# Optimization experiments

Hardware: AMD Instinct MI355X
Metric: run time of the kernel (lower is better)

The kernel has to match this reference:

```python
import math
import jax
import jax.numpy as jnp
import numpy as np

B, N = 64, 64
R = N * (N - 1)
DIST_THRESH = 0.35


def _pair_indices(n):
    # edge e = i*(n-1) + j - (j > i): row-major over i, ascending j skipping j == i
    ii = np.repeat(np.arange(n), n - 1)
    jm = np.tile(np.arange(n), (n, 1))
    jj = jm[~np.eye(n, dtype=bool)].reshape(-1)
    return ii, jj


def _rot_basis(a):
    # a: [..., 1] angle -> [..., 2, 2] rotation basis rows [cos,sin],[cos(a+pi/2),sin(a+pi/2)]
    first = jnp.concatenate([jnp.cos(a), jnp.sin(a)], axis=-1)
    second = jnp.concatenate([jnp.cos(a + math.pi / 2), jnp.sin(a + math.pi / 2)], axis=-1)
    return jnp.stack([first, second], axis=-2)


def setup_inputs() -> dict:
    ks = jax.random.split(jax.random.key(0), 8)
    nrm = lambda k, shape, s=1.0: (jax.random.normal(k, shape) * s).astype(jnp.float32)
    return dict(
        objects_state=jax.random.uniform(ks[0], (B, N, 8), dtype=jnp.float32),
        objects_shape=nrm(ks[1], (B, N, 10)),
        relation_info=nrm(ks[2], (B, R, 3)),
        s_mean=jnp.zeros((8,), jnp.float32), s_std=jnp.ones((8,), jnp.float32),
        sh_mean=jnp.zeros((10,), jnp.float32), sh_std=jnp.ones((10,), jnp.float32),
        v_mean=jnp.zeros((3,), jnp.float32), v_std=jnp.ones((3,), jnp.float32),
        W1=nrm(ks[3], (32, 256), 32 ** -0.5), b1=jnp.zeros((256,), jnp.float32),
        W2=nrm(ks[4], (256, 128), 256 ** -0.5), b2=jnp.zeros((128,), jnp.float32),
        W3=nrm(ks[5], (141, 256), 141 ** -0.5), b3=jnp.zeros((256,), jnp.float32),
        W4=nrm(ks[6], (256, 3), 256 ** -0.5), b4=jnp.zeros((3,), jnp.float32),
    )


def reference(objects_state, objects_shape, relation_info, s_mean, s_std, sh_mean, sh_std,
              v_mean, v_std, W1, b1, W2, b2, W3, b3, W4, b4):
    n = objects_state.shape[1]
    ii, jj = _pair_indices(n)

    # ---- pre_proces: distance-threshold edge build into dense one-hot matrices ----
    pos = objects_state[:, :, 0:2]
    dist = jnp.sqrt(jnp.sum((pos[:, :, None, :] - pos[:, None, :, :]) ** 2, axis=-1))
    # torch: where(dist<0.35, dist, 0).nonzero() -> keeps dist<0.35 AND dist != 0 (drops self-edges)
    mask = ((dist < DIST_THRESH) & (dist != 0.0)).astype(jnp.float32)
    mask_flat = mask[:, ii, jj]  # [B, R]
    eye = jnp.eye(n, dtype=jnp.float32)
    receiver_relations = mask_flat[:, :, None] * eye[ii][None]  # [B, R, N]
    sender_relations = mask_flat[:, :, None] * eye[jj][None]    # [B, R, N]

    data_state = (objects_state - s_mean) / s_std
    data_shape = (objects_shape - sh_mean) / sh_std

    senders_state = jnp.einsum('brn,bnd->brd', sender_relations, data_state)
    receivers_state = jnp.einsum('brn,bnd->brd', receiver_relations, data_state)
    senders_shape = jnp.einsum('brn,bnd->brd', sender_relations, data_shape)
    receivers_shape = jnp.einsum('brn,bnd->brd', receiver_relations, data_shape)

    basis = _rot_basis(receivers_state[:, :, 2:3])  # [B, R, 2, 2]
    diff_state = senders_state - receivers_state
    temp = jnp.stack([diff_state[:, :, 0:2], diff_state[:, :, 3:5], senders_state[:, :, 6:8]], axis=-1)  # [B,R,2,3]
    tfed = jnp.einsum('brij,brjk->brik', basis, temp)  # [B,R,2,3]
    angle_diff = diff_state[:, :, 2:3]
    diff_feat = jnp.concatenate([
        tfed[:, :, :, 0], tfed[:, :, :, 1], tfed[:, :, :, 2],
        jnp.sin(2 * angle_diff), jnp.cos(2 * angle_diff),
        diff_state[:, :, 5:6],
    ], axis=-1)  # [B, R, 9]
    rel_data = jnp.concatenate([relation_info, diff_feat, receivers_shape, senders_shape], axis=-1)  # [B,R,32]

    obj_basis = _rot_basis(data_state[:, :, 2:3])  # [B, N, 2, 2]
    obj_vel_tfed = jnp.einsum('bnij,bnj->bni', obj_basis, data_state[:, :, 3:5])
    obj_data = jnp.concatenate([obj_vel_tfed, data_state[:, :, 5:6], data_shape], axis=-1)  # [B,N,13]

    # ---- interaction-network Net ----
    effects = jax.nn.relu(rel_data @ W1 + b1) @ W2 + b2  # [B, R, 128]
    agg = jnp.einsum('brn,bre->bne', receiver_relations, effects)  # [B, N, 128]
    out_vel = jax.nn.relu(jnp.concatenate([obj_data, agg], axis=-1) @ W3 + b3) @ W4 + b4  # [B,N,3]

    # ---- post_proces ----
    angles = objects_state[:, 1:, 2:3]
    pred = out_vel[:, 1:, :] * v_std + v_mean  # inv_transform_vel
    basis_back = _rot_basis(-angles)
    vel_back = jnp.einsum('bnij,bnj->bni', basis_back, pred[:, :, :2])
    x_dot = jnp.concatenate([vel_back, pred[:, :, 2:]], axis=-1)  # [B, N-1, 3]

    tp = np.eye(6, dtype=np.float32)
    tp[3:, 3:] = 0.0
    tq = np.zeros((3, 6), dtype=np.float32)
    for i in range(3):
        tq[i, i] = 1.0
        tq[i, 3 + i] = 1.0
    x_next = objects_state[:, 1:, :6] @ jnp.asarray(tp) + x_dot @ jnp.asarray(tq)
    return x_next  # [B, N-1, 6]
```

## Files before the change

### kernel.cpp

```cpp
#include <hip/hip_runtime.h>
#include <math.h>

#define BB 64
#define NN 64
#define NM1 63
#define RR (NN*(NN-1))

#define WS1_OFF 0
#define WS2_OFF 16384
#define WS3_OFF 81920
#define WSH_OFF 163840
#define WSC_OFF 2260992

typedef short bf16x8 __attribute__((ext_vector_type(8)));
typedef float f32x4 __attribute__((ext_vector_type(4)));
union U4 { uint4 u; bf16x8 b; };

__device__ inline unsigned int f2bf(float f) {
    unsigned int u = __float_as_uint(f);
    return (u + 0x7FFFu + ((u >> 16) & 1u)) >> 16;
}
__device__ inline unsigned int pack2(float a, float b) {
    return f2bf(a) | (f2bf(b) << 16);
}

__global__ __launch_bounds__(64) void pack_kernel(
    const float* __restrict__ W1, const float* __restrict__ W2,
    const float* __restrict__ W3, unsigned char* __restrict__ ws)
{
    const int u = blockIdx.x, l = threadIdx.x;
    const int col16 = l & 15, quad = l >> 4;
    float v[8];
    uint4* dst;
    if (u < 16) {
        const int nt = u, col = nt*16 + col16;
        #pragma unroll
        for (int j = 0; j < 8; ++j) {
            const int k = quad*8 + j;
            const int orig = k < 12 ? k : (k < 22 ? k+10 : k-10);
            v[j] = W1[orig*256 + col];
        }
        dst = (uint4*)(ws + WS1_OFF) + (nt*64 + l);
    } else if (u < 80) {
        const int w = u-16, nt = w >> 3, kc = w & 7, col = nt*16 + col16;
        #pragma unroll
        for (int j = 0; j < 8; ++j) {
            const int k = kc*32 + quad*8 + j;
            v[j] = W2[(size_t)k*128 + col];
        }
        dst = (uint4*)(ws + WS2_OFF) + ((nt*8 + kc)*64 + l);
    } else {
        const int w = u-80, nt = w/5, kc = w - nt*5, col = nt*16 + col16;
        #pragma unroll
        for (int j = 0; j < 8; ++j) {
            const int k = kc*32 + quad*8 + j;
            v[j] = (k < 141) ? W3[(size_t)k*256 + col] : 0.f;
        }
        dst = (uint4*)(ws + WS3_OFF) + ((nt*5 + kc)*64 + l);
    }
    uint4 o;
    o.x = pack2(v[0], v[1]); o.y = pack2(v[2], v[3]);
    o.z = pack2(v[4], v[5]); o.w = pack2(v[6], v[7]);
    *dst = o;
}

__global__ __launch_bounds__(256) void rel_kernel(
    const float* __restrict__ objects_state,
    const float* __restrict__ objects_shape,
    const float* __restrict__ relation_info,
    const float* __restrict__ s_mean, const float* __restrict__ s_std,
    const float* __restrict__ sh_mean, const float* __restrict__ sh_std,
    const float* __restrict__ b1,
    unsigned char* __restrict__ ws)
{
    __shared__ float s_posx[64], s_posy[64];
    __shared__ float s_rst[4][8];
    __shared__ float s_rsh[4][12];
    __shared__ int   s_cntg[4];
    __shared__ float s_nst[64][9];
    __shared__ float s_nsh[64][11];
    __shared__ __align__(16) unsigned int relb_w[256*20];
    __shared__ float s_hsum[4][256];

    const int b  = blockIdx.x >> 4;
    const int nb = (blockIdx.x & 15) * 4;
    const int t  = threadIdx.x;
    const int wv = t >> 6, lane = t & 63, col16 = lane & 15, quad = lane >> 4;

    if (t < 64) {
        s_posx[t] = objects_state[(size_t)(b*NN+t)*8 + 0];
        s_posy[t] = objects_state[(size_t)(b*NN+t)*8 + 1];
    }
    if (t >= 64 && t < 96) {
        int g = (t-64) >> 3, c = t & 7;
        s_rst[g][c] = (objects_state[(size_t)(b*NN+nb+g)*8 + c] - s_mean[c]) / s_std[c];
    }
    if (t >= 96 && t < 136) {
        int idx = t-96, g = idx/10, c = idx - g*10;
        s_rsh[g][c] = (objects_shape[(size_t)(b*NN+nb+g)*10 + c] - sh_mean[c]) / sh_std[c];
    }
    if (t >= 136 && t < 140) s_cntg[t-136] = 0;
    #pragma unroll
    for (int r = 0; r < 2; ++r) {
        int idx = t + r*256, o = idx >> 3, c = idx & 7;
        s_nst[o][c] = (objects_state[(size_t)(b*NN+o)*8 + c] - s_mean[c]) / s_std[c];
    }
    #pragma unroll
    for (int r = 0; r < 3; ++r) {
        int idx = t + r*256;
        if (idx < 640) {
            int o = idx/10, c = idx - o*10;
            s_nsh[o][c] = (objects_shape[(size_t)(b*NN+o)*10 + c] - sh_mean[c]) / sh_std[c];
        }
    }
    __syncthreads();

    if (t < 252) {
        const int g = t/63, k = t - g*63, n = nb + g, j = k + (k >= n);
        const float dx = s_posx[n] - s_posx[j];
        const float dy = s_posy[n] - s_posy[j];
        const float dist = sqrtf(dx*dx + dy*dy);
        if (dist < 0.35f && dist != 0.0f) {
            const int slot = atomicAdd(&s_cntg[g], 1);
            const int row = g*64 + slot;
            float f[32];
            const size_t rb = ((size_t)b*RR + n*NM1 + k)*3;
            f[0] = relation_info[rb];
            f[1] = relation_info[rb+1];
            f[2] = relation_info[rb+2];
            float sd[8];
            #pragma unroll
            for (int c = 0; c < 8; ++c) sd[c] = s_nst[j][c];
            const float rd0 = s_rst[g][0], rd1 = s_rst[g][1], rd2 = s_rst[g][2],
                        rd3 = s_rst[g][3], rd4 = s_rst[g][4], rd5 = s_rst[g][5];
            const float d0 = sd[0]-rd0, d1 = sd[1]-rd1, d2 = sd[2]-rd2,
                        d3 = sd[3]-rd3, d4 = sd[4]-rd4, d5 = sd[5]-rd5;
            const float ca = cosf(rd2), sa = sinf(rd2);
            f[3]  =  ca*d0 + sa*d1;
            f[4]  = -sa*d0 + ca*d1;
            f[5]  =  ca*d3 + sa*d4;
            f[6]  = -sa*d3 + ca*d4;
            f[7]  =  ca*sd[6] + sa*sd[7];
            f[8]  = -sa*sd[6] + ca*sd[7];
            f[9]  = sinf(2.f*d2);
            f[10] = cosf(2.f*d2);
            f[11] = d5;
            #pragma unroll
            for (int c = 0; c < 10; ++c) f[12+c] = s_nsh[j][c];
            #pragma unroll
            for (int c = 0; c < 10; ++c) f[22+c] = s_rsh[g][c];
            uint4* dst = (uint4*)&relb_w[row*20];
            #pragma unroll
            for (int w4 = 0; w4 < 4; ++w4) {
                uint4 o;
                o.x = pack2(f[w4*8+0], f[w4*8+1]);
                o.y = pack2(f[w4*8+2], f[w4*8+3]);
                o.z = pack2(f[w4*8+4], f[w4*8+5]);
                o.w = pack2(f[w4*8+6], f[w4*8+7]);
                dst[w4] = o;
            }
        }
    }
    __syncthreads();

    {
        int cg[4];
        #pragma unroll
        for (int g = 0; g < 4; ++g) cg[g] = s_cntg[g];
        const uint4* w1f = (const uint4*)(ws + WS1_OFF);
        #pragma unroll
        for (int q4 = 0; q4 < 4; ++q4) {
            const int nt = wv*4 + q4, col = nt*16 + col16;
            U4 bu; bu.u = w1f[nt*64 + lane];
            const float b1v = b1[col];
            float hs[4] = {0.f, 0.f, 0.f, 0.f};
            #pragma unroll
            for (int g = 0; g < 4; ++g) {
                const int mts = (cg[g] + 15) >> 4;
                for (int mt = 0; mt < mts; ++mt) {
                    U4 au; au.u = *(const uint4*)&relb_w[(g*64 + mt*16 + col16)*20 + quad*4];
                    f32x4 acc = {0.f, 0.f, 0.f, 0.f};
                    acc = __builtin_amdgcn_mfma_f32_16x16x32_bf16(au.b, bu.b, acc, 0, 0, 0);
                    const int rb2 = mt*16 + quad*4;
                    #pragma unroll
                    for (int i = 0; i < 4; ++i) {
                        const float vv = fmaxf(acc[i] + b1v, 0.f);
                        hs[g] += (rb2 + i < cg[g]) ? vv : 0.f;
                    }
                }
            }
            #pragma unroll
            for (int g = 0; g < 4; ++g) {
                float vv = hs[g];
                vv += __shfl_xor(vv, 16);
                vv += __shfl_xor(vv, 32);
                if (quad == 0) s_hsum[g][col] = vv;
            }
        }
    }
    __syncthreads();

    {
        unsigned int* hdst = (unsigned int*)(ws + WSH_OFF);
        #pragma unroll
        for (int r = 0; r < 2; ++r) {
            const int idx = r*256 + t, g = idx >> 7, i = idx & 127;
            const int obj = b*NN + nb + g;
            hdst[obj*128 + i] = pack2(s_hsum[g][2*i], s_hsum[g][2*i+1]);
        }
        if (t < 4) ((int*)(ws + WSC_OFF))[b*NN + nb + t] = s_cntg[t];
    }
}

__global__ __launch_bounds__(256) void obj_kernel(
    const float* __restrict__ objects_state,
    const float* __restrict__ objects_shape,
    const float* __restrict__ s_mean, const float* __restrict__ s_std,
    const float* __restrict__ sh_mean, const float* __restrict__ sh_std,
    const float* __restrict__ v_mean, const float* __restrict__ v_std,
    const float* __restrict__ b2, const float* __restrict__ b3,
    const float* __restrict__ W4, const float* __restrict__ b4,
    const unsigned char* __restrict__ ws,
    float* __restrict__ out)
{
    __shared__ __align__(16) unsigned short s_q[16*168];
    __shared__ float s_red[4][16][3];
    __shared__ float s_outv[16][3];

    const int bi = blockIdx.x >> 2, ot = blockIdx.x & 3;
    const int obj0 = bi*NN + ot*16;
    const int t = threadIdx.x, wv = t >> 6, lane = t & 63,
              col16 = lane & 15, quad = lane >> 4;

    #pragma unroll
    for (int r = 0; r < 2; ++r) {
        const int idx = r*256 + t;
        if (idx < 432) {
            const int m = idx/27, c = 141 + (idx - m*27);
            s_q[m*168 + c] = 0;
        }
    }

    if (t >= 64 && t < 80) {
        const int o = t - 64, n = ot*16 + o;
        const size_t sb = (size_t)(bi*NN + n)*8;
        const float rd2 = (objects_state[sb+2] - s_mean[2]) / s_std[2];
        const float rd3 = (objects_state[sb+3] - s_mean[3]) / s_std[3];
        const float rd4 = (objects_state[sb+4] - s_mean[4]) / s_std[4];
        const float rd5 = (objects_state[sb+5] - s_mean[5]) / s_std[5];
        const float ca = cosf(rd2), sa = sinf(rd2);
        s_q[o*168 + 0] = (unsigned short)f2bf( ca*rd3 + sa*rd4);
        s_q[o*168 + 1] = (unsigned short)f2bf(-sa*rd3 + ca*rd4);
        s_q[o*168 + 2] = (unsigned short)f2bf(rd5);
        #pragma unroll
        for (int c = 0; c < 10; ++c)
            s_q[o*168 + 3 + c] = (unsigned short)f2bf(
                (objects_shape[(size_t)(bi*NN+n)*10 + c] - sh_mean[c]) / sh_std[c]);
    }

    {
        const uint4* hsrc = (const uint4*)(ws + WSH_OFF);
        U4 af[8];
        #pragma unroll
        for (int kc = 0; kc < 8; ++kc)
            af[kc].u = hsrc[(size_t)(obj0 + col16)*32 + kc*4 + quad];
        float cntv[4];
        #pragma unroll
        for (int i = 0; i < 4; ++i)
            cntv[i] = (float)((const int*)(ws + WSC_OFF))[obj0 + quad*4 + i];
        const uint4* w2f = (const uint4*)(ws + WS2_OFF);
        #pragma unroll
        for (int ntl = 0; ntl < 2; ++ntl) {
            const int nt = wv*2 + ntl, col = nt*16 + col16;
            f32x4 acc = {0.f, 0.f, 0.f, 0.f};
            #pragma unroll
            for (int kc = 0; kc < 8; ++kc) {
                U4 bu; bu.u = w2f[(nt*8 + kc)*64 + lane];
                acc = __builtin_amdgcn_mfma_f32_16x16x32_bf16(af[kc].b, bu.b, acc, 0, 0, 0);
            }
            const float b2v = b2[col];
            #pragma unroll
            for (int i = 0; i < 4; ++i) {
                const int row = quad*4 + i;
                s_q[row*168 + 13 + col] = (unsigned short)f2bf(acc[i] + cntv[i]*b2v);
            }
        }
    }
    __syncthreads();

    {
        U4 af3[5];
        #pragma unroll
        for (int kc = 0; kc < 5; ++kc)
            af3[kc].u = *(const uint4*)&s_q[col16*168 + kc*32 + quad*8];
        const uint4* w3f = (const uint4*)(ws + WS3_OFF);
        float p[4][3];
        #pragma unroll
        for (int i = 0; i < 4; ++i) { p[i][0]=0.f; p[i][1]=0.f; p[i][2]=0.f; }
        #pragma unroll
        for (int ntl = 0; ntl < 4; ++ntl) {
            const int nt = wv*4 + ntl, col = nt*16 + col16;
            f32x4 acc = {0.f, 0.f, 0.f, 0.f};
            #pragma unroll
            for (int kc = 0; kc < 5; ++kc) {
                U4 bu; bu.u = w3f[(nt*5 + kc)*64 + lane];
                acc = __builtin_amdgcn_mfma_f32_16x16x32_bf16(af3[kc].b, bu.b, acc, 0, 0, 0);
            }
            const float b3v = b3[col];
            const float w40 = W4[col*3+0], w41 = W4[col*3+1], w42 = W4[col*3+2];
            #pragma unroll
            for (int i = 0; i < 4; ++i) {
                const float h = fmaxf(acc[i] + b3v, 0.f);
                p[i][0] = fmaf(h, w40, p[i][0]);
                p[i][1] = fmaf(h, w41, p[i][1]);
                p[i][2] = fmaf(h, w42, p[i][2]);
            }
        }
        #pragma unroll
        for (int off = 1; off < 16; off <<= 1)
            #pragma unroll
            for (int i = 0; i < 4; ++i) {
                p[i][0] += __shfl_xor(p[i][0], off);
                p[i][1] += __shfl_xor(p[i][1], off);
                p[i][2] += __shfl_xor(p[i][2], off);
            }
        if (col16 == 0)
            #pragma unroll
            for (int i = 0; i < 4; ++i) {
                s_red[wv][quad*4+i][0] = p[i][0];
                s_red[wv][quad*4+i][1] = p[i][1];
                s_red[wv][quad*4+i][2] = p[i][2];
            }
    }
    __syncthreads();
    if (t < 48) {
        const int m = t/3, o = t - m*3;
        s_outv[m][o] = b4[o] + s_red[0][m][o] + s_red[1][m][o]
                             + s_red[2][m][o] + s_red[3][m][o];
    }
    __syncthreads();

    if (t < 96) {
        const int m = t/6, i = t - m*6, n = ot*16 + m;
        if (n >= 1) {
            const float q0 = s_outv[m][0]*v_std[0] + v_mean[0];
            const float q1 = s_outv[m][1]*v_std[1] + v_mean[1];
            const float q2 = s_outv[m][2]*v_std[2] + v_mean[2];
            const float ang = objects_state[(size_t)(bi*NN+n)*8 + 2];
            const float ca = cosf(ang), sa = sinf(ang);
            const float xd0 = ca*q0 - sa*q1;
            const float xd1 = sa*q0 + ca*q1;
            const int im = i % 3;
            const float xd = (im == 0) ? xd0 : (im == 1) ? xd1 : q2;
            const float base = (i < 3) ? objects_state[(size_t)(bi*NN+n)*8 + i] : 0.f;
            out[((size_t)bi*NM1 + (n-1))*6 + i] = base + xd;
        }
    }
}

extern "C" void kernel_launch(void* const* d_in, const int* in_sizes, int n_in,
                              void* d_out, int out_size, void* d_ws, size_t ws_size,
                              hipStream_t stream) {
    const float* objects_state = (const float*)d_in[0];
    const float* objects_shape = (const float*)d_in[1];
    const float* relation_info = (const float*)d_in[2];
    const float* s_mean  = (const float*)d_in[3];
    const float* s_std   = (const float*)d_in[4];
    const float* sh_mean = (const float*)d_in[5];
    const float* sh_std  = (const float*)d_in[6];
    const float* v_mean  = (const float*)d_in[7];
    const float* v_std   = (const float*)d_in[8];
    const float* W1 = (const float*)d_in[9];
    const float* b1 = (const float*)d_in[10];
    const float* W2 = (const float*)d_in[11];
    const float* b2 = (const float*)d_in[12];
    const float* W3 = (const float*)d_in[13];
    const float* b3 = (const float*)d_in[14];
    const float* W4 = (const float*)d_in[15];
    const float* b4 = (const float*)d_in[16];
    unsigned char* ws = (unsigned char*)d_ws;

    pack_kernel<<<dim3(160), dim3(64), 0, stream>>>(W1, W2, W3, ws);
    rel_kernel<<<dim3(BB*16), dim3(256), 0, stream>>>(
        objects_state, objects_shape, relation_info,
        s_mean, s_std, sh_mean, sh_std, b1, ws);
    obj_kernel<<<dim3(BB*4), dim3(256), 0, stream>>>(
        objects_state, objects_shape,
        s_mean, s_std, sh_mean, sh_std, v_mean, v_std,
        b2, b3, W4, b4, ws, (float*)d_out);
}
```

Baseline: 109.6 us.

## Fuse relation and object kernels into one per-batch main kernel with per-object precompute

Merges the relation-MLP kernel and the object-MLP kernel into a single kernel, so each block handles 8 receivers and keeps the aggregated hidden sums in shared memory instead of round-tripping them through global workspace. A new prep kernel packs the weights and also precomputes per-object normalized features and rotation sin/cos into a 112-byte record. The main kernel reads these records and relation_info into LDS up front, and skips the per-row validity mask by subtracting a padding correction. The trade-offs are larger blocks, more LDS per block, and half of the MFMA rows in the object stage doing unused work.

```diff
diff --git a/kernel.cpp b/kernel.cpp
--- a/kernel.cpp
+++ b/kernel.cpp
@@ -9,8 +9,7 @@
 #define WS1_OFF 0
 #define WS2_OFF 16384
 #define WS3_OFF 81920
-#define WSH_OFF 163840
-#define WSC_OFF 2260992
+#define WSO_OFF 163840
 
 typedef short bf16x8 __attribute__((ext_vector_type(8)));
 typedef float f32x4 __attribute__((ext_vector_type(4)));
@@ -24,132 +23,151 @@
     return f2bf(a) | (f2bf(b) << 16);
 }
 
-__global__ __launch_bounds__(64) void pack_kernel(
+__global__ __launch_bounds__(256) void prep_kernel(
+    const float* __restrict__ objects_state,
+    const float* __restrict__ objects_shape,
+    const float* __restrict__ s_mean, const float* __restrict__ s_std,
+    const float* __restrict__ sh_mean, const float* __restrict__ sh_std,
     const float* __restrict__ W1, const float* __restrict__ W2,
     const float* __restrict__ W3, unsigned char* __restrict__ ws)
 {
-    const int u = blockIdx.x, l = threadIdx.x;
-    const int col16 = l & 15, quad = l >> 4;
-    float v[8];
-    uint4* dst;
-    if (u < 16) {
-        const int nt = u, col = nt*16 + col16;
-        #pragma unroll
-        for (int j = 0; j < 8; ++j) {
-            const int k = quad*8 + j;
-            const int orig = k < 12 ? k : (k < 22 ? k+10 : k-10);
-            v[j] = W1[orig*256 + col];
-        }
-        dst = (uint4*)(ws + WS1_OFF) + (nt*64 + l);
-    } else if (u < 80) {
-        const int w = u-16, nt = w >> 3, kc = w & 7, col = nt*16 + col16;
-        #pragma unroll
-        for (int j = 0; j < 8; ++j) {
-            const int k = kc*32 + quad*8 + j;
-            v[j] = W2[(size_t)k*128 + col];
-        }
-        dst = (uint4*)(ws + WS2_OFF) + ((nt*8 + kc)*64 + l);
+    const int t = threadIdx.x;
+    if (blockIdx.x < 40) {
+        const int u = blockIdx.x*4 + (t >> 6), l = t & 63;
+        const int col16 = l & 15, quad = l >> 4;
+        float v[8];
+        uint4* dst;
+        if (u < 16) {
+            const int nt = u, col = nt*16 + col16;
+            #pragma unroll
+            for (int j = 0; j < 8; ++j) {
+                const int k = quad*8 + j;
+                const int orig = k < 12 ? k : (k < 22 ? k+10 : k-10);
+                v[j] = W1[orig*256 + col];
+            }
+            dst = (uint4*)(ws + WS1_OFF) + (nt*64 + l);
+        } else if (u < 80) {
+            const int w = u-16, nt = w >> 3, kc = w & 7, col = nt*16 + col16;
+            #pragma unroll
+            for (int j = 0; j < 8; ++j)
+                v[j] = W2[(size_t)(kc*32 + quad*8 + j)*128 + col];
+            dst = (uint4*)(ws + WS2_OFF) + ((nt*8 + kc)*64 + l);
+        } else {
+            const int w = u-80, nt = w/5, kc = w - nt*5, col = nt*16 + col16;
+            #pragma unroll
+            for (int j = 0; j < 8; ++j) {
+                const int k = kc*32 + quad*8 + j;
+                v[j] = (k < 141) ? W3[(size_t)k*256 + col] : 0.f;
+            }
+            dst = (uint4*)(ws + WS3_OFF) + ((nt*5 + kc)*64 + l);
+        }
+        uint4 o;
+        o.x = pack2(v[0], v[1]); o.y = pack2(v[2], v[3]);
+        o.z = pack2(v[4], v[5]); o.w = pack2(v[6], v[7]);
+        *dst = o;
     } else {
-        const int w = u-80, nt = w/5, kc = w - nt*5, col = nt*16 + col16;
-        #pragma unroll
-        for (int j = 0; j < 8; ++j) {
-            const int k = kc*32 + quad*8 + j;
-            v[j] = (k < 141) ? W3[(size_t)k*256 + col] : 0.f;
-        }
-        dst = (uint4*)(ws + WS3_OFF) + ((nt*5 + kc)*64 + l);
-    }
-    uint4 o;
-    o.x = pack2(v[0], v[1]); o.y = pack2(v[2], v[3]);
-    o.z = pack2(v[4], v[5]); o.w = pack2(v[6], v[7]);
-    *dst = o;
-}
-
-__global__ __launch_bounds__(256) void rel_kernel(
-    const float* __restrict__ objects_state,
-    const float* __restrict__ objects_shape,
+        const int obj = (blockIdx.x - 40)*256 + t;
+        float st[8], sh[10];
+        #pragma unroll
+        for (int c = 0; c < 8; ++c)  st[c] = objects_state[(size_t)obj*8 + c];
+        #pragma unroll
+        for (int c = 0; c < 10; ++c) sh[c] = objects_shape[(size_t)obj*10 + c];
+        float f[28];
+        f[0] = st[0]; f[1] = st[1]; f[26] = st[2]; f[27] = 0.f;
+        #pragma unroll
+        for (int c = 0; c < 8; ++c)  f[2+c]  = (st[c] - s_mean[c]) / s_std[c];
+        #pragma unroll
+        for (int c = 0; c < 10; ++c) f[10+c] = (sh[c] - sh_mean[c]) / sh_std[c];
+        float sa, ca, sr, cr;
+        __sincosf(f[4], &sa, &ca);
+        __sincosf(st[2], &sr, &cr);
+        sa = sinf(f[4]); ca = cosf(f[4]);
+        sr = sinf(st[2]); cr = cosf(st[2]);
+        f[20] = ca; f[21] = sa; f[22] = cr; f[23] = sr;
+        f[24] =  ca*f[5] + sa*f[6];
+        f[25] = -sa*f[5] + ca*f[6];
+        float4* dst = (float4*)(ws + WSO_OFF + (size_t)obj*112);
+        #pragma unroll
+        for (int q = 0; q < 7; ++q)
+            dst[q] = make_float4(f[q*4], f[q*4+1], f[q*4+2], f[q*4+3]);
+    }
+}
+
+__global__ __launch_bounds__(512) void main_kernel(
     const float* __restrict__ relation_info,
-    const float* __restrict__ s_mean, const float* __restrict__ s_std,
-    const float* __restrict__ sh_mean, const float* __restrict__ sh_std,
-    const float* __restrict__ b1,
-    unsigned char* __restrict__ ws)
+    const float* __restrict__ v_mean, const float* __restrict__ v_std,
+    const float* __restrict__ b1, const float* __restrict__ b2,
+    const float* __restrict__ b3,
+    const float* __restrict__ W4, const float* __restrict__ b4,
+    const unsigned char* __restrict__ ws,
+    float* __restrict__ out)
 {
-    __shared__ float s_posx[64], s_posy[64];
-    __shared__ float s_rst[4][8];
-    __shared__ float s_rsh[4][12];
-    __shared__ int   s_cntg[4];
-    __shared__ float s_nst[64][9];
-    __shared__ float s_nsh[64][11];
-    __shared__ __align__(16) unsigned int relb_w[256*20];
-    __shared__ float s_hsum[4][256];
-
-    const int b  = blockIdx.x >> 4;
-    const int nb = (blockIdx.x & 15) * 4;
+    __shared__ __align__(16) float P[64][28];
+    __shared__ __align__(16) unsigned int relb_w[8*64*16];
+    __shared__ __align__(16) float RI[1512];
+    __shared__ __align__(16) unsigned short s_h[16*264];
+    __shared__ __align__(16) unsigned short s_q[16*168];
+    __shared__ int   s_cntg[8];
+    __shared__ float s_red[8][16][3];
+    __shared__ float s_outv[16][3];
+
+    const int b  = blockIdx.x >> 3;
+    const int nb = (blockIdx.x & 7) * 8;
     const int t  = threadIdx.x;
     const int wv = t >> 6, lane = t & 63, col16 = lane & 15, quad = lane >> 4;
 
-    if (t < 64) {
-        s_posx[t] = objects_state[(size_t)(b*NN+t)*8 + 0];
-        s_posy[t] = objects_state[(size_t)(b*NN+t)*8 + 1];
-    }
-    if (t >= 64 && t < 96) {
-        int g = (t-64) >> 3, c = t & 7;
-        s_rst[g][c] = (objects_state[(size_t)(b*NN+nb+g)*8 + c] - s_mean[c]) / s_std[c];
-    }
-    if (t >= 96 && t < 136) {
-        int idx = t-96, g = idx/10, c = idx - g*10;
-        s_rsh[g][c] = (objects_shape[(size_t)(b*NN+nb+g)*10 + c] - sh_mean[c]) / sh_std[c];
-    }
-    if (t >= 136 && t < 140) s_cntg[t-136] = 0;
-    #pragma unroll
-    for (int r = 0; r < 2; ++r) {
-        int idx = t + r*256, o = idx >> 3, c = idx & 7;
-        s_nst[o][c] = (objects_state[(size_t)(b*NN+o)*8 + c] - s_mean[c]) / s_std[c];
-    }
-    #pragma unroll
-    for (int r = 0; r < 3; ++r) {
-        int idx = t + r*256;
-        if (idx < 640) {
-            int o = idx/10, c = idx - o*10;
-            s_nsh[o][c] = (objects_shape[(size_t)(b*NN+o)*10 + c] - sh_mean[c]) / sh_std[c];
-        }
-    }
-    __syncthreads();
-
-    if (t < 252) {
+    {
+        uint4 z = make_uint4(0,0,0,0);
+        uint4* relb4 = (uint4*)relb_w;
+        #pragma unroll
+        for (int r = 0; r < 4; ++r) relb4[r*512 + t] = z;
+        if (t < 336) ((uint4*)s_q)[t] = z;
+        if (t < 8) s_cntg[t] = 0;
+        const float* psrc = (const float*)(ws + WSO_OFF + (size_t)(b*64)*112);
+        float* P0 = &P[0][0];
+        #pragma unroll
+        for (int r = 0; r < 4; ++r) {
+            const int idx = r*512 + t;
+            if (idx < 1792) P0[idx] = psrc[idx];
+        }
+        const float* rsrc = relation_info + ((size_t)b*RR + nb*NM1)*3;
+        #pragma unroll
+        for (int r = 0; r < 3; ++r) {
+            const int idx = r*512 + t;
+            if (idx < 1512) RI[idx] = rsrc[idx];
+        }
+    }
+    __syncthreads();
+
+    if (t < 504) {
         const int g = t/63, k = t - g*63, n = nb + g, j = k + (k >= n);
-        const float dx = s_posx[n] - s_posx[j];
-        const float dy = s_posy[n] - s_posy[j];
+        const float dx = P[n][0] - P[j][0];
+        const float dy = P[n][1] - P[j][1];
         const float dist = sqrtf(dx*dx + dy*dy);
         if (dist < 0.35f && dist != 0.0f) {
             const int slot = atomicAdd(&s_cntg[g], 1);
-            const int row = g*64 + slot;
+            const int row = (g << 6) + slot;
             float f[32];
-            const size_t rb = ((size_t)b*RR + n*NM1 + k)*3;
-            f[0] = relation_info[rb];
-            f[1] = relation_info[rb+1];
-            f[2] = relation_info[rb+2];
-            float sd[8];
-            #pragma unroll
-            for (int c = 0; c < 8; ++c) sd[c] = s_nst[j][c];
-            const float rd0 = s_rst[g][0], rd1 = s_rst[g][1], rd2 = s_rst[g][2],
-                        rd3 = s_rst[g][3], rd4 = s_rst[g][4], rd5 = s_rst[g][5];
-            const float d0 = sd[0]-rd0, d1 = sd[1]-rd1, d2 = sd[2]-rd2,
-                        d3 = sd[3]-rd3, d4 = sd[4]-rd4, d5 = sd[5]-rd5;
-            const float ca = cosf(rd2), sa = sinf(rd2);
+            f[0] = RI[t*3]; f[1] = RI[t*3+1]; f[2] = RI[t*3+2];
+            const float rd0 = P[n][2], rd1 = P[n][3], rd2 = P[n][4],
+                        rd3 = P[n][5], rd4 = P[n][6], rd5 = P[n][7];
+            const float ca = P[n][20], sa = P[n][21];
+            const float d0 = P[j][2]-rd0, d1 = P[j][3]-rd1, d2 = P[j][4]-rd2,
+                        d3 = P[j][5]-rd3, d4 = P[j][6]-rd4, d5 = P[j][7]-rd5;
             f[3]  =  ca*d0 + sa*d1;
             f[4]  = -sa*d0 + ca*d1;
             f[5]  =  ca*d3 + sa*d4;
             f[6]  = -sa*d3 + ca*d4;
-            f[7]  =  ca*sd[6] + sa*sd[7];
-            f[8]  = -sa*sd[6] + ca*sd[7];
+            f[7]  =  ca*P[j][8] + sa*P[j][9];
+            f[8]  = -sa*P[j][8] + ca*P[j][9];
             f[9]  = sinf(2.f*d2);
             f[10] = cosf(2.f*d2);
             f[11] = d5;
             #pragma unroll
-            for (int c = 0; c < 10; ++c) f[12+c] = s_nsh[j][c];
-            #pragma unroll
-            for (int c = 0; c < 10; ++c) f[22+c] = s_rsh[g][c];
-            uint4* dst = (uint4*)&relb_w[row*20];
+            for (int c = 0; c < 10; ++c) f[12+c] = P[j][10+c];
+            #pragma unroll
+            for (int c = 0; c < 10; ++c) f[22+c] = P[n][10+c];
+            uint4* dst = (uint4*)&relb_w[row*16];
             #pragma unroll
             for (int w4 = 0; w4 < 4; ++w4) {
                 uint4 o;
@@ -164,126 +182,83 @@
     __syncthreads();
 
     {
-        int cg[4];
-        #pragma unroll
-        for (int g = 0; g < 4; ++g) cg[g] = s_cntg[g];
+        int cg[8];
+        #pragma unroll
+        for (int g = 0; g < 8; ++g) cg[g] = s_cntg[g];
         const uint4* w1f = (const uint4*)(ws + WS1_OFF);
-        #pragma unroll
-        for (int q4 = 0; q4 < 4; ++q4) {
-            const int nt = wv*4 + q4, col = nt*16 + col16;
-            U4 bu; bu.u = w1f[nt*64 + lane];
-            const float b1v = b1[col];
-            float hs[4] = {0.f, 0.f, 0.f, 0.f};
-            #pragma unroll
-            for (int g = 0; g < 4; ++g) {
-                const int mts = (cg[g] + 15) >> 4;
-                for (int mt = 0; mt < mts; ++mt) {
-                    U4 au; au.u = *(const uint4*)&relb_w[(g*64 + mt*16 + col16)*20 + quad*4];
-                    f32x4 acc = {0.f, 0.f, 0.f, 0.f};
-                    acc = __builtin_amdgcn_mfma_f32_16x16x32_bf16(au.b, bu.b, acc, 0, 0, 0);
-                    const int rb2 = mt*16 + quad*4;
-                    #pragma unroll
-                    for (int i = 0; i < 4; ++i) {
-                        const float vv = fmaxf(acc[i] + b1v, 0.f);
-                        hs[g] += (rb2 + i < cg[g]) ? vv : 0.f;
-                    }
+        U4 bu0, bu1;
+        bu0.u = w1f[(wv*2+0)*64 + lane];
+        bu1.u = w1f[(wv*2+1)*64 + lane];
+        const float b10 = b1[(wv*2+0)*16 + col16];
+        const float b11 = b1[(wv*2+1)*16 + col16];
+        float hs0[8], hs1[8];
+        #pragma unroll
+        for (int g = 0; g < 8; ++g) { hs0[g] = 0.f; hs1[g] = 0.f; }
+        #pragma unroll
+        for (int g = 0; g < 8; ++g) {
+            const int mts = (cg[g] + 15) >> 4;
+            for (int mt = 0; mt < mts; ++mt) {
+                U4 au;
+                au.u = *(const uint4*)&relb_w[((g<<6) + mt*16 + col16)*16 + quad*4];
+                f32x4 a0 = {0.f,0.f,0.f,0.f}, a1 = {0.f,0.f,0.f,0.f};
+                a0 = __builtin_amdgcn_mfma_f32_16x16x32_bf16(au.b, bu0.b, a0, 0,0,0);
+                a1 = __builtin_amdgcn_mfma_f32_16x16x32_bf16(au.b, bu1.b, a1, 0,0,0);
+                #pragma unroll
+                for (int i = 0; i < 4; ++i) {
+                    hs0[g] += fmaxf(a0[i] + b10, 0.f);
+                    hs1[g] += fmaxf(a1[i] + b11, 0.f);
                 }
             }
-            #pragma unroll
-            for (int g = 0; g < 4; ++g) {
-                float vv = hs[g];
-                vv += __shfl_xor(vv, 16);
-                vv += __shfl_xor(vv, 32);
-                if (quad == 0) s_hsum[g][col] = vv;
-            }
-        }
-    }
-    __syncthreads();
-
+        }
+        const float rb0 = fmaxf(b10, 0.f), rb1 = fmaxf(b11, 0.f);
+        #pragma unroll
+        for (int g = 0; g < 8; ++g) {
+            const int mts = (cg[g] + 15) >> 4;
+            const float pad = (float)(mts*16 - cg[g]);
+            float v0 = hs0[g], v1 = hs1[g];
+            v0 += __shfl_xor(v0, 16); v0 += __shfl_xor(v0, 32);
+            v1 += __shfl_xor(v1, 16); v1 += __shfl_xor(v1, 32);
+            if (quad == 0) {
+                s_h[g*264 + (wv*2+0)*16 + col16] =
+                    (unsigned short)f2bf(v0 - pad*rb0);
+                s_h[g*264 + (wv*2+1)*16 + col16] =
+                    (unsigned short)f2bf(v1 - pad*rb1);
+            }
+        }
+    }
+    __syncthreads();
+
+    if (t < 104) {
+        const int m = t/13, c = t - m*13, n = nb + m;
+        float v;
+        if (c == 0) v = P[n][24];
+        else if (c == 1) v = P[n][25];
+        else if (c == 2) v = P[n][7];
+        else v = P[n][10 + c - 3];
+        s_q[m*168 + c] = (unsigned short)f2bf(v);
+    }
     {
-        unsigned int* hdst = (unsigned int*)(ws + WSH_OFF);
-        #pragma unroll
-        for (int r = 0; r < 2; ++r) {
-            const int idx = r*256 + t, g = idx >> 7, i = idx & 127;
-            const int obj = b*NN + nb + g;
-            hdst[obj*128 + i] = pack2(s_hsum[g][2*i], s_hsum[g][2*i+1]);
-        }
-        if (t < 4) ((int*)(ws + WSC_OFF))[b*NN + nb + t] = s_cntg[t];
-    }
-}
-
-__global__ __launch_bounds__(256) void obj_kernel(
-    const float* __restrict__ objects_state,
-    const float* __restrict__ objects_shape,
-    const float* __restrict__ s_mean, const float* __restrict__ s_std,
-    const float* __restrict__ sh_mean, const float* __restrict__ sh_std,
-    const float* __restrict__ v_mean, const float* __restrict__ v_std,
-    const float* __restrict__ b2, const float* __restrict__ b3,
-    const float* __restrict__ W4, const float* __restrict__ b4,
-    const unsigned char* __restrict__ ws,
-    float* __restrict__ out)
-{
-    __shared__ __align__(16) unsigned short s_q[16*168];
-    __shared__ float s_red[4][16][3];
-    __shared__ float s_outv[16][3];
-
-    const int bi = blockIdx.x >> 2, ot = blockIdx.x & 3;
-    const int obj0 = bi*NN + ot*16;
-    const int t = threadIdx.x, wv = t >> 6, lane = t & 63,
-              col16 = lane & 15, quad = lane >> 4;
-
-    #pragma unroll
-    for (int r = 0; r < 2; ++r) {
-        const int idx = r*256 + t;
-        if (idx < 432) {
-            const int m = idx/27, c = 141 + (idx - m*27);
-            s_q[m*168 + c] = 0;
-        }
-    }
-
-    if (t >= 64 && t < 80) {
-        const int o = t - 64, n = ot*16 + o;
-        const size_t sb = (size_t)(bi*NN + n)*8;
-        const float rd2 = (objects_state[sb+2] - s_mean[2]) / s_std[2];
-        const float rd3 = (objects_state[sb+3] - s_mean[3]) / s_std[3];
-        const float rd4 = (objects_state[sb+4] - s_mean[4]) / s_std[4];
-        const float rd5 = (objects_state[sb+5] - s_mean[5]) / s_std[5];
-        const float ca = cosf(rd2), sa = sinf(rd2);
-        s_q[o*168 + 0] = (unsigned short)f2bf( ca*rd3 + sa*rd4);
-        s_q[o*168 + 1] = (unsigned short)f2bf(-sa*rd3 + ca*rd4);
-        s_q[o*168 + 2] = (unsigned short)f2bf(rd5);
-        #pragma unroll
-        for (int c = 0; c < 10; ++c)
-            s_q[o*168 + 3 + c] = (unsigned short)f2bf(
-                (objects_shape[(size_t)(bi*NN+n)*10 + c] - sh_mean[c]) / sh_std[c]);
-    }
-
-    {
-        const uint4* hsrc = (const uint4*)(ws + WSH_OFF);
         U4 af[8];
         #pragma unroll
         for (int kc = 0; kc < 8; ++kc)
-            af[kc].u = hsrc[(size_t)(obj0 + col16)*32 + kc*4 + quad];
+            af[kc].u = *(const uint4*)&s_h[(lane & 15)*264 + kc*32 + quad*8];
         float cntv[4];
         #pragma unroll
         for (int i = 0; i < 4; ++i)
-            cntv[i] = (float)((const int*)(ws + WSC_OFF))[obj0 + quad*4 + i];
+            cntv[i] = (float)s_cntg[(quad*4 + i) & 7];
         const uint4* w2f = (const uint4*)(ws + WS2_OFF);
-        #pragma unroll
-        for (int ntl = 0; ntl < 2; ++ntl) {
-            const int nt = wv*2 + ntl, col = nt*16 + col16;
-            f32x4 acc = {0.f, 0.f, 0.f, 0.f};
-            #pragma unroll
-            for (int kc = 0; kc < 8; ++kc) {
-                U4 bu; bu.u = w2f[(nt*8 + kc)*64 + lane];
-                acc = __builtin_amdgcn_mfma_f32_16x16x32_bf16(af[kc].b, bu.b, acc, 0, 0, 0);
-            }
-            const float b2v = b2[col];
-            #pragma unroll
-            for (int i = 0; i < 4; ++i) {
-                const int row = quad*4 + i;
-                s_q[row*168 + 13 + col] = (unsigned short)f2bf(acc[i] + cntv[i]*b2v);
-            }
+        f32x4 acc = {0.f,0.f,0.f,0.f};
+        #pragma unroll
+        for (int kc = 0; kc < 8; ++kc) {
+            U4 bu; bu.u = w2f[(wv*8 + kc)*64 + lane];
+            acc = __builtin_amdgcn_mfma_f32_16x16x32_bf16(af[kc].b, bu.b, acc, 0,0,0);
+        }
+        const float b2v = b2[wv*16 + col16];
+        #pragma unroll
+        for (int i = 0; i < 4; ++i) {
+            const int row = quad*4 + i;
+            s_q[row*168 + 13 + wv*16 + col16] =
+                (unsigned short)f2bf(acc[i] + cntv[i]*b2v);
         }
     }
     __syncthreads();
@@ -292,19 +267,19 @@
         U4 af3[5];
         #pragma unroll
         for (int kc = 0; kc < 5; ++kc)
-            af3[kc].u = *(const uint4*)&s_q[col16*168 + kc*32 + quad*8];
+            af3[kc].u = *(const uint4*)&s_q[(lane & 15)*168 + kc*32 + quad*8];
         const uint4* w3f = (const uint4*)(ws + WS3_OFF);
         float p[4][3];
         #pragma unroll
         for (int i = 0; i < 4; ++i) { p[i][0]=0.f; p[i][1]=0.f; p[i][2]=0.f; }
         #pragma unroll
-        for (int ntl = 0; ntl < 4; ++ntl) {
-            const int nt = wv*4 + ntl, col = nt*16 + col16;
-            f32x4 acc = {0.f, 0.f, 0.f, 0.f};
+        for (int ntl = 0; ntl < 2; ++ntl) {
+            const int nt = wv + ntl*8, col = nt*16 + col16;
+            f32x4 acc = {0.f,0.f,0.f,0.f};
             #pragma unroll
             for (int kc = 0; kc < 5; ++kc) {
                 U4 bu; bu.u = w3f[(nt*5 + kc)*64 + lane];
-                acc = __builtin_amdgcn_mfma_f32_16x16x32_bf16(af3[kc].b, bu.b, acc, 0, 0, 0);
+                acc = __builtin_amdgcn_mfma_f32_16x16x32_bf16(af3[kc].b, bu.b, acc, 0,0,0);
             }
             const float b3v = b3[col];
             const float w40 = W4[col*3+0], w41 = W4[col*3+1], w42 = W4[col*3+2];
@@ -335,25 +310,29 @@
     __syncthreads();
     if (t < 48) {
         const int m = t/3, o = t - m*3;
-        s_outv[m][o] = b4[o] + s_red[0][m][o] + s_red[1][m][o]
-                             + s_red[2][m][o] + s_red[3][m][o];
-    }
-    __syncthreads();
-
-    if (t < 96) {
-        const int m = t/6, i = t - m*6, n = ot*16 + m;
+        float acc = b4[o];
+        #pragma unroll
+        for (int w = 0; w < 8; ++w) acc += s_red[w][m][o];
+        s_outv[m][o] = acc;
+    }
+    __syncthreads();
+
+    if (t < 48) {
+        const int m = t/6, i = t - m*6, n = nb + m;
         if (n >= 1) {
             const float q0 = s_outv[m][0]*v_std[0] + v_mean[0];
             const float q1 = s_outv[m][1]*v_std[1] + v_mean[1];
             const float q2 = s_outv[m][2]*v_std[2] + v_mean[2];
-            const float ang = objects_state[(size_t)(bi*NN+n)*8 + 2];
-            const float ca = cosf(ang), sa = sinf(ang);
-            const float xd0 = ca*q0 - sa*q1;
-            const float xd1 = sa*q0 + ca*q1;
+            const float cr = P[n][22], sr = P[n][23];
+            const float xd0 = cr*q0 - sr*q1;
+            const float xd1 = sr*q0 + cr*q1;
             const int im = i % 3;
             const float xd = (im == 0) ? xd0 : (im == 1) ? xd1 : q2;
-            const float base = (i < 3) ? objects_state[(size_t)(bi*NN+n)*8 + i] : 0.f;
-            out[((size_t)bi*NM1 + (n-1))*6 + i] = base + xd;
+            float base = 0.f;
+            if (i == 0) base = P[n][0];
+            else if (i == 1) base = P[n][1];
+            else if (i == 2) base = P[n][26];
+            out[((size_t)b*NM1 + (n-1))*6 + i] = base + xd;
         }
     }
 }
@@ -380,12 +359,10 @@
     const float* b4 = (const float*)d_in[16];
     unsigned char* ws = (unsigned char*)d_ws;
 
-    pack_kernel<<<dim3(160), dim3(64), 0, stream>>>(W1, W2, W3, ws);
-    rel_kernel<<<dim3(BB*16), dim3(256), 0, stream>>>(
-        objects_state, objects_shape, relation_info,
-        s_mean, s_std, sh_mean, sh_std, b1, ws);
-    obj_kernel<<<dim3(BB*4), dim3(256), 0, stream>>>(
-        objects_state, objects_shape,
-        s_mean, s_std, sh_mean, sh_std, v_mean, v_std,
-        b2, b3, W4, b4, ws, (float*)d_out);
-}
+    prep_kernel<<<dim3(56), dim3(256), 0, stream>>>(
+        objects_state, objects_shape, s_mean, s_std, sh_mean, sh_std,
+        W1, W2, W3, ws);
+    main_kernel<<<dim3(BB*8), dim3(512), 0, stream>>>(
+        relation_info, v_mean, v_std, b1, b2, b3, W4, b4,
+        ws, (float*)d_out);
+}
```

After: 105.6 us, median of 2. 3.6% less time.
